# Kernel tuning notes

Measured on AMD Instinct MI355X. Metric: run time of the kernel, lower is better.

The kernel has to match this reference:

```python
import jax, jax.numpy as jnp
import numpy as np

NUM_STEPS = 151            # num_steps from __init__
STEP = 2.0 / (NUM_STEPS - 1)
HALF = (NUM_STEPS - 1) // 2  # bin offset: t_j = -1 + j*STEP, 1/STEP = HALF
N = 4096
D = 512
NUM_CLASSES = 751


def _soft_histogram(s, mask, size):
    # Triangular-kernel (linear) soft binning, equivalent to the original
    # indsa/indsb masked-repeat construction: each similarity s in
    # [t_{j-1}, t_j] contributes (1-frac) to bin j-1 and frac to bin j.
    x = s / STEP
    k = jnp.floor(x)           # zero-gradient, plays the role of s_repeat_floor
    frac = x - k               # (s - (t_j - STEP)) / STEP
    kI = k.astype(jnp.int32)
    idx_lo = jnp.clip(kI + HALF, 0, NUM_STEPS - 1)
    idx_hi = jnp.clip(kI + HALF + 1, 0, NUM_STEPS - 1)
    hist = jnp.zeros((NUM_STEPS,), dtype=s.dtype)
    hist = hist.at[idx_lo].add((1.0 - frac) * mask)
    hist = hist.at[idx_hi].add(frac * mask)
    return hist / size


def setup_inputs() -> dict:
    key = jax.random.key(0)
    kf, kc = jax.random.split(key)
    return {
        "features": jax.random.normal(kf, (N, D), dtype=jnp.float32),
        "classes": jax.random.randint(kc, (N,), 0, NUM_CLASSES, dtype=jnp.int32),
    }


def reference(features, classes):
    # L2Normalization
    f = features / jnp.linalg.norm(features, axis=1, keepdims=True)
    dists = f @ f.T                                   # [N, N] cosine sims
    iu, ju = np.triu_indices(features.shape[0], 1)    # static upper-tri pairs
    s = dists[iu, ju]                                 # [P] P = N(N-1)/2
    pos = (classes[iu] == classes[ju]).astype(s.dtype)
    neg = 1.0 - pos
    hist_pos = _soft_histogram(s, pos, jnp.sum(pos))
    hist_neg = _soft_histogram(s, neg, jnp.sum(neg))
    cdf_pos = jnp.cumsum(hist_pos)                    # tril-masked column sums == cumsum
    return jnp.sum(hist_neg * cdf_pos)
```

## Files before the change

### kernel.cpp

```cpp
#include <hip/hip_runtime.h>
#include <math.h>

#define N 4096
#define D 512
#define NUM_STEPS 151
#define HALF_BINS 75
#define INV_STEP 75.0f
#define NUM_CLASSES 751
#define P_TOTAL 8386560.0f

#define WS_SUM_ALL 0
#define WS_POS_CNT 1
#define WS_SUM_POS 2
#define WS_S_POS   3
#define WS_DONE2   4
#define WS_DONE3   5
#define WS_G_OFF   8
#define WS_H_OFF   160
#define WS_LIST_OFF 1024
#define MAXP (1 << 18)
#define WS_FEAT_OFF (WS_LIST_OFF + MAXP)
#define WS_FEATB_OFF (WS_FEAT_OFF + N * D)
#define WS_IDX_OFF  (WS_FEATB_OFF + N * D / 2)
#define WS_OFFS_OFF (WS_IDX_OFF + N)
#define WS_POFF_OFF (WS_OFFS_OFF + NUM_CLASSES + 1)

#define POS_BLOCKS 512

typedef __bf16 bf16x8 __attribute__((ext_vector_type(8)));
typedef float floatx4 __attribute__((ext_vector_type(4)));

__global__ __launch_bounds__(256) void k_norm_sort(const float* __restrict__ feat,
                                                   const int* __restrict__ cls,
                                                   float* __restrict__ nf,
                                                   __bf16* __restrict__ nfb,
                                                   int* __restrict__ pairList,
                                                   float* __restrict__ wsf,
                                                   int* __restrict__ wsi) {
    int t = threadIdx.x;
    if (blockIdx.x > 0) {
        int row = blockIdx.x - 1;
        const float* fr = feat + (size_t)row * D;
        float a = fr[t];
        float b = fr[t + 256];
        float ss = a * a + b * b;
        for (int o = 32; o > 0; o >>= 1) ss += __shfl_down(ss, o, 64);
        __shared__ float wsum[4];
        int lane = t & 63, wid = t >> 6;
        if (lane == 0) wsum[wid] = ss;
        __syncthreads();
        float tot = wsum[0] + wsum[1] + wsum[2] + wsum[3];
        float inv = 1.0f / sqrtf(tot);
        float na = a * inv, nb = b * inv;
        nf[(size_t)row * D + t] = na;
        nf[(size_t)row * D + t + 256] = nb;
        nfb[(size_t)row * D + t] = (__bf16)na;
        nfb[(size_t)row * D + t + 256] = (__bf16)nb;
        return;
    }

    if (t == 0) {
        wsf[WS_SUM_ALL] = 0.f;
        wsf[WS_SUM_POS] = 0.f;
        wsi[WS_DONE2] = 0;
        wsi[WS_DONE3] = 0;
    }
    {
        float* histG = wsf + WS_H_OFF;
        for (int b = t; b < NUM_STEPS; b += 256) histG[b] = 0.f;
    }
    __shared__ int hcnt[NUM_CLASSES];
    __shared__ int hoff[NUM_CLASSES];
    __shared__ int poff[NUM_CLASSES];
    __shared__ int ridx[N];
    __shared__ int wsumR[4], wsumP[4];
    for (int c = t; c < NUM_CLASSES; c += 256) hcnt[c] = 0;
    __syncthreads();
    for (int n = t; n < N; n += 256) atomicAdd(&hcnt[cls[n]], 1);
    __syncthreads();

    int c0 = t * 3;
    int cntPreR[3], cntPreP[3];
    int myR = 0, myP = 0;
    #pragma unroll
    for (int k = 0; k < 3; ++k) {
        int c = c0 + k;
        int cnt = (c < NUM_CLASSES) ? hcnt[c] : 0;
        cntPreR[k] = myR; cntPreP[k] = myP;
        myR += cnt;
        myP += cnt * (cnt - 1) / 2;
    }
    int lane = t & 63, wv = t >> 6;
    int incR = myR, incP = myP;
    for (int o = 1; o < 64; o <<= 1) {
        int rr = __shfl_up(incR, o, 64);
        int pp = __shfl_up(incP, o, 64);
        if (lane >= o) { incR += rr; incP += pp; }
    }
    if (lane == 63) { wsumR[wv] = incR; wsumP[wv] = incP; }
    __syncthreads();
    int baseR = 0, baseP = 0;
    for (int w = 0; w < wv; ++w) { baseR += wsumR[w]; baseP += wsumP[w]; }
    int exR = baseR + incR - myR;
    int exP = baseP + incP - myP;
    #pragma unroll
    for (int k = 0; k < 3; ++k) {
        int c = c0 + k;
        if (c < NUM_CLASSES) { hoff[c] = exR + cntPreR[k]; poff[c] = exP + cntPreP[k]; }
    }
    __syncthreads();

    for (int c = t; c < NUM_CLASSES; c += 256) hcnt[c] = hoff[c];
    __syncthreads();
    for (int n = t; n < N; n += 256) {
        int p = atomicAdd(&hcnt[cls[n]], 1);
        ridx[p] = n;
    }
    __syncthreads();

    #pragma unroll
    for (int k = 0; k < 3; ++k) {
        int c = c0 + k;
        if (c >= NUM_CLASSES) continue;
        int o0 = hoff[c];
        int nc = hcnt[c] - o0;
        int pB = poff[c];
        int q = 0;
        for (int a = 0; a < nc - 1; ++a) {
            int ri = ridx[o0 + a];
            for (int b = a + 1; b < nc; ++b) {
                int rj = ridx[o0 + b];
                if (pB + q < MAXP) pairList[pB + q] = (ri << 12) | rj;
                ++q;
            }
        }
    }
    if (t == 0) {
        int totP = wsumP[0] + wsumP[1] + wsumP[2] + wsumP[3];
        wsi[WS_POS_CNT] = totP;
    }
}

__global__ __launch_bounds__(256) void k_pos_cdf(const float* __restrict__ nf,
                                                 const int* __restrict__ pairList,
                                                 float* __restrict__ histG,
                                                 float* __restrict__ G,
                                                 float* __restrict__ wsf,
                                                 int* __restrict__ wsi) {
    __shared__ float hloc[NUM_STEPS];
    int t = threadIdx.x;
    int lane = t & 63;
    int wave = t >> 6;
    for (int b = t; b < NUM_STEPS; b += 256) hloc[b] = 0.f;
    __syncthreads();

    int totP = wsi[WS_POS_CNT];
    if (totP > MAXP) totP = MAXP;
    const int STRIDE = POS_BLOCKS * 4;
    int p = blockIdx.x * 4 + wave;
    int vNext = (p < totP) ? pairList[p] : 0;
    for (; p < totP; p += STRIDE) {
        int v = vNext;
        int pn = p + STRIDE;
        if (pn < totP) vNext = pairList[pn];
        int ri = v >> 12, rj = v & 4095;
        const float4* x4 = (const float4*)(nf + (size_t)ri * D);
        const float4* y4 = (const float4*)(nf + (size_t)rj * D);
        float4 xa = x4[lane * 2], xb = x4[lane * 2 + 1];
        float4 ya = y4[lane * 2], yb = y4[lane * 2 + 1];
        float s = xa.x * ya.x + xa.y * ya.y + xa.z * ya.z + xa.w * ya.w
                + xb.x * yb.x + xb.y * yb.y + xb.z * yb.z + xb.w * yb.w;
        for (int o = 32; o > 0; o >>= 1) s += __shfl_down(s, o, 64);
        if (lane == 0) {
            float x = s * INV_STEP;
            float kf = floorf(x);
            float frac = x - kf;
            int kI = (int)kf;
            int lo = min(max(kI + HALF_BINS, 0), NUM_STEPS - 1);
            int hi = min(max(kI + HALF_BINS + 1, 0), NUM_STEPS - 1);
            atomicAdd(&hloc[lo], 1.0f - frac);
            atomicAdd(&hloc[hi], frac);
        }
    }
    __syncthreads();
    for (int b = t; b < NUM_STEPS; b += 256) {
        float v = hloc[b];
        if (v != 0.f) atomicAdd(&histG[b], v);
    }

    __shared__ bool sdone;
    __syncthreads();
    if (t == 0) {
        __threadfence();
        int v = atomicAdd(&wsi[WS_DONE2], 1);
        sdone = (v == (int)gridDim.x - 1);
    }
    __syncthreads();
    if (!sdone) return;

    __shared__ float sc[2][NUM_STEPS];
    float hv = 0.f;
    if (t < NUM_STEPS) {
        hv = atomicAdd(&histG[t], 0.0f);
        sc[0][t] = hv;
    }
    __syncthreads();
    int src = 0;
    for (int o = 1; o < NUM_STEPS; o <<= 1) {
        if (t < NUM_STEPS) {
            float v = sc[src][t];
            if (t >= o) v += sc[src][t - o];
            sc[1 - src][t] = v;
        }
        __syncthreads();
        src ^= 1;
    }
    float invC = (totP > 0) ? (1.0f / (float)totP) : 0.f;
    float prod = 0.f;
    if (t < NUM_STEPS) {
        float g = sc[src][t] * invC;
        G[t] = g;
        prod = hv * g;
    }
    for (int o = 32; o > 0; o >>= 1) prod += __shfl_down(prod, o, 64);
    __shared__ float wsum[4];
    if ((t & 63) == 0) wsum[t >> 6] = prod;
    __syncthreads();
    if (t == 0) {
        wsf[WS_SUM_POS] = wsum[0] + wsum[1] + wsum[2] + wsum[3];
        wsf[WS_S_POS] = (float)totP;
    }
}

#define TILES_1D 32
#define LDSS 40

__global__ __launch_bounds__(256) void k_gram_final(const __bf16* __restrict__ nfb,
                                                    const float* __restrict__ G,
                                                    float* __restrict__ wsf,
                                                    int* __restrict__ wsi,
                                                    float* __restrict__ out) {
    int bid = blockIdx.x;
    int ti = 0, rem = bid;
    while (rem >= TILES_1D - ti) { rem -= TILES_1D - ti; ++ti; }
    int tj = ti + rem;

    __shared__ __align__(16) __bf16 As[128 * LDSS];
    __shared__ __align__(16) __bf16 Bs[128 * LDSS];
    __shared__ float Gs[NUM_STEPS];

    int tid = threadIdx.x;
    for (int b = tid; b < NUM_STEPS; b += 256) Gs[b] = G[b];

    int lane = tid & 63;
    int wave = tid >> 6;
    int wm = (wave >> 1) * 64;
    int wn = (wave & 1) * 64;
    int fr = lane & 15;
    int fk = (lane >> 4) * 8;

    int rowA0 = ti * 128, rowB0 = tj * 128;

    floatx4 acc[4][4] = {};

    int e0 = tid * 8;
    int e1 = e0 + 2048;
    int r0 = e0 >> 5, c0 = e0 & 31;
    int r1 = e1 >> 5, c1 = e1 & 31;

    for (int kb = 0; kb < D / 32; ++kb) {
        int kbase = kb * 32;
        *(float4*)(&As[r0 * LDSS + c0]) = *(const float4*)(nfb + (size_t)(rowA0 + r0) * D + kbase + c0);
        *(float4*)(&As[r1 * LDSS + c1]) = *(const float4*)(nfb + (size_t)(rowA0 + r1) * D + kbase + c1);
        *(float4*)(&Bs[r0 * LDSS + c0]) = *(const float4*)(nfb + (size_t)(rowB0 + r0) * D + kbase + c0);
        *(float4*)(&Bs[r1 * LDSS + c1]) = *(const float4*)(nfb + (size_t)(rowB0 + r1) * D + kbase + c1);
        __syncthreads();

        bf16x8 a[4], b[4];
        #pragma unroll
        for (int r = 0; r < 4; ++r)
            a[r] = *(const bf16x8*)(&As[(wm + r * 16 + fr) * LDSS + fk]);
        #pragma unroll
        for (int c = 0; c < 4; ++c)
            b[c] = *(const bf16x8*)(&Bs[(wn + c * 16 + fr) * LDSS + fk]);

        #pragma unroll
        for (int r = 0; r < 4; ++r)
            #pragma unroll
            for (int c = 0; c < 4; ++c)
                acc[r][c] = __builtin_amdgcn_mfma_f32_16x16x32_bf16(a[r], b[c], acc[r][c], 0, 0, 0);
        __syncthreads();
    }

    int crow = (lane >> 4) * 4;
    int ccol = lane & 15;
    float gsum = 0.f;
    #pragma unroll
    for (int r = 0; r < 4; ++r) {
        #pragma unroll
        for (int c = 0; c < 4; ++c) {
            #pragma unroll
            for (int reg = 0; reg < 4; ++reg) {
                int gi = rowA0 + wm + r * 16 + crow + reg;
                int gj = rowB0 + wn + c * 16 + ccol;
                if (gi < gj) {
                    float s = acc[r][c][reg];
                    float x = s * INV_STEP;
                    float kf = floorf(x);
                    float frac = x - kf;
                    int kI = (int)kf;
                    int lo = min(max(kI + HALF_BINS, 0), NUM_STEPS - 1);
                    int hi = min(max(kI + HALF_BINS + 1, 0), NUM_STEPS - 1);
                    gsum += (1.f - frac) * Gs[lo] + frac * Gs[hi];
                }
            }
        }
    }
    for (int o = 32; o > 0; o >>= 1) gsum += __shfl_down(gsum, o, 64);
    __shared__ float wsum[4];
    if ((tid & 63) == 0) wsum[tid >> 6] = gsum;
    __syncthreads();
    if (tid == 0) atomicAdd(&wsf[WS_SUM_ALL], wsum[0] + wsum[1] + wsum[2] + wsum[3]);

    __shared__ bool sdone;
    if (tid == 0) {
        __threadfence();
        int v = atomicAdd(&wsi[WS_DONE3], 1);
        sdone = (v == (int)gridDim.x - 1);
    }
    __syncthreads();
    if (sdone && tid == 0) {
        __threadfence();
        float sAll = atomicAdd(&wsf[WS_SUM_ALL], 0.0f);
        float C = wsf[WS_S_POS];
        float sneg = P_TOTAL - C;
        out[0] = (sAll - wsf[WS_SUM_POS]) / sneg;
    }
}

extern "C" void kernel_launch(void* const* d_in, const int* in_sizes, int n_in,
                              void* d_out, int out_size, void* d_ws, size_t ws_size,
                              hipStream_t stream) {
    const float* feat = (const float*)d_in[0];
    const int* cls = (const int*)d_in[1];
    float* out = (float*)d_out;
    float* wsf = (float*)d_ws;
    int* wsi = (int*)d_ws;

    float* nf = wsf + WS_FEAT_OFF;
    __bf16* nfb = (__bf16*)(wsf + WS_FEATB_OFF);
    int* pairList = wsi + WS_LIST_OFF;
    float* G = wsf + WS_G_OFF;
    float* histG = wsf + WS_H_OFF;

    k_norm_sort<<<N + 1, 256, 0, stream>>>(feat, cls, nf, nfb, pairList, wsf, wsi);
    k_pos_cdf<<<POS_BLOCKS, 256, 0, stream>>>(nf, pairList, histG, G, wsf, wsi);
    int nTiles = TILES_1D * (TILES_1D + 1) / 2;
    k_gram_final<<<nTiles, 256, 0, stream>>>(nfb, G, wsf, wsi, out);
}
```

Before: 140.0 us.

## Fuse positive-pair histogram and Gram pass into one kernel via all-pair histogram

```diff
diff --git a/kernel.cpp b/kernel.cpp
--- a/kernel.cpp
+++ b/kernel.cpp
@@ -15,17 +15,16 @@
 #define WS_S_POS   3
 #define WS_DONE2   4
 #define WS_DONE3   5
-#define WS_G_OFF   8
-#define WS_H_OFF   160
+#define WS_HP_OFF  8
+#define WS_HA_OFF  160
 #define WS_LIST_OFF 1024
 #define MAXP (1 << 18)
 #define WS_FEAT_OFF (WS_LIST_OFF + MAXP)
 #define WS_FEATB_OFF (WS_FEAT_OFF + N * D)
-#define WS_IDX_OFF  (WS_FEATB_OFF + N * D / 2)
-#define WS_OFFS_OFF (WS_IDX_OFF + N)
-#define WS_POFF_OFF (WS_OFFS_OFF + NUM_CLASSES + 1)
-
-#define POS_BLOCKS 512
+
+#define TILES_1D 32
+#define NTILES (TILES_1D * (TILES_1D + 1) / 2)
+#define LDSS 40
 
 typedef __bf16 bf16x8 __attribute__((ext_vector_type(8)));
 typedef float floatx4 __attribute__((ext_vector_type(4)));
@@ -66,8 +65,10 @@
         wsi[WS_DONE3] = 0;
     }
     {
-        float* histG = wsf + WS_H_OFF;
-        for (int b = t; b < NUM_STEPS; b += 256) histG[b] = 0.f;
+        for (int b = t; b < NUM_STEPS; b += 256) {
+            wsf[WS_HP_OFF + b] = 0.f;
+            wsf[WS_HA_OFF + b] = 0.f;
+        }
     }
     __shared__ int hcnt[NUM_CLASSES];
     __shared__ int hoff[NUM_CLASSES];
@@ -141,119 +142,67 @@
     }
 }
 
-__global__ __launch_bounds__(256) void k_pos_cdf(const float* __restrict__ nf,
-                                                 const int* __restrict__ pairList,
-                                                 float* __restrict__ histG,
-                                                 float* __restrict__ G,
-                                                 float* __restrict__ wsf,
-                                                 int* __restrict__ wsi) {
+__global__ __launch_bounds__(256) void k_pair_gram(const float* __restrict__ nf,
+                                                   const __bf16* __restrict__ nfb,
+                                                   const int* __restrict__ pairList,
+                                                   float* __restrict__ histPosG,
+                                                   float* __restrict__ histAllG,
+                                                   float* __restrict__ wsf,
+                                                   int* __restrict__ wsi,
+                                                   float* __restrict__ out) {
+    __shared__ __align__(16) __bf16 As[128 * LDSS];
+    __shared__ __align__(16) __bf16 Bs[128 * LDSS];
     __shared__ float hloc[NUM_STEPS];
-    int t = threadIdx.x;
-    int lane = t & 63;
-    int wave = t >> 6;
-    for (int b = t; b < NUM_STEPS; b += 256) hloc[b] = 0.f;
+    __shared__ float hAll[NUM_STEPS];
+
+    int tid = threadIdx.x;
+    int lane = tid & 63;
+    int wave = tid >> 6;
+
+    for (int b = tid; b < NUM_STEPS; b += 256) { hloc[b] = 0.f; hAll[b] = 0.f; }
     __syncthreads();
 
     int totP = wsi[WS_POS_CNT];
     if (totP > MAXP) totP = MAXP;
-    const int STRIDE = POS_BLOCKS * 4;
-    int p = blockIdx.x * 4 + wave;
-    int vNext = (p < totP) ? pairList[p] : 0;
-    for (; p < totP; p += STRIDE) {
-        int v = vNext;
-        int pn = p + STRIDE;
-        if (pn < totP) vNext = pairList[pn];
-        int ri = v >> 12, rj = v & 4095;
-        const float4* x4 = (const float4*)(nf + (size_t)ri * D);
-        const float4* y4 = (const float4*)(nf + (size_t)rj * D);
-        float4 xa = x4[lane * 2], xb = x4[lane * 2 + 1];
-        float4 ya = y4[lane * 2], yb = y4[lane * 2 + 1];
-        float s = xa.x * ya.x + xa.y * ya.y + xa.z * ya.z + xa.w * ya.w
-                + xb.x * yb.x + xb.y * yb.y + xb.z * yb.z + xb.w * yb.w;
-        for (int o = 32; o > 0; o >>= 1) s += __shfl_down(s, o, 64);
-        if (lane == 0) {
-            float x = s * INV_STEP;
-            float kf = floorf(x);
-            float frac = x - kf;
-            int kI = (int)kf;
-            int lo = min(max(kI + HALF_BINS, 0), NUM_STEPS - 1);
-            int hi = min(max(kI + HALF_BINS + 1, 0), NUM_STEPS - 1);
-            atomicAdd(&hloc[lo], 1.0f - frac);
-            atomicAdd(&hloc[hi], frac);
-        }
-    }
-    __syncthreads();
-    for (int b = t; b < NUM_STEPS; b += 256) {
+    {
+        const int STRIDE = NTILES * 4;
+        int p = blockIdx.x * 4 + wave;
+        int vNext = (p < totP) ? pairList[p] : 0;
+        for (; p < totP; p += STRIDE) {
+            int v = vNext;
+            int pn = p + STRIDE;
+            if (pn < totP) vNext = pairList[pn];
+            int ri = v >> 12, rj = v & 4095;
+            const float4* x4 = (const float4*)(nf + (size_t)ri * D);
+            const float4* y4 = (const float4*)(nf + (size_t)rj * D);
+            float4 xa = x4[lane * 2], xb = x4[lane * 2 + 1];
+            float4 ya = y4[lane * 2], yb = y4[lane * 2 + 1];
+            float s = xa.x * ya.x + xa.y * ya.y + xa.z * ya.z + xa.w * ya.w
+                    + xb.x * yb.x + xb.y * yb.y + xb.z * yb.z + xb.w * yb.w;
+            for (int o = 32; o > 0; o >>= 1) s += __shfl_down(s, o, 64);
+            if (lane == 0) {
+                float x = s * INV_STEP;
+                float kf = floorf(x);
+                float frac = x - kf;
+                int kI = (int)kf;
+                int lo = min(max(kI + HALF_BINS, 0), NUM_STEPS - 1);
+                int hi = min(max(kI + HALF_BINS + 1, 0), NUM_STEPS - 1);
+                atomicAdd(&hloc[lo], 1.0f - frac);
+                atomicAdd(&hloc[hi], frac);
+            }
+        }
+    }
+    __syncthreads();
+    for (int b = tid; b < NUM_STEPS; b += 256) {
         float v = hloc[b];
-        if (v != 0.f) atomicAdd(&histG[b], v);
-    }
-
-    __shared__ bool sdone;
-    __syncthreads();
-    if (t == 0) {
-        __threadfence();
-        int v = atomicAdd(&wsi[WS_DONE2], 1);
-        sdone = (v == (int)gridDim.x - 1);
-    }
-    __syncthreads();
-    if (!sdone) return;
-
-    __shared__ float sc[2][NUM_STEPS];
-    float hv = 0.f;
-    if (t < NUM_STEPS) {
-        hv = atomicAdd(&histG[t], 0.0f);
-        sc[0][t] = hv;
-    }
-    __syncthreads();
-    int src = 0;
-    for (int o = 1; o < NUM_STEPS; o <<= 1) {
-        if (t < NUM_STEPS) {
-            float v = sc[src][t];
-            if (t >= o) v += sc[src][t - o];
-            sc[1 - src][t] = v;
-        }
-        __syncthreads();
-        src ^= 1;
-    }
-    float invC = (totP > 0) ? (1.0f / (float)totP) : 0.f;
-    float prod = 0.f;
-    if (t < NUM_STEPS) {
-        float g = sc[src][t] * invC;
-        G[t] = g;
-        prod = hv * g;
-    }
-    for (int o = 32; o > 0; o >>= 1) prod += __shfl_down(prod, o, 64);
-    __shared__ float wsum[4];
-    if ((t & 63) == 0) wsum[t >> 6] = prod;
-    __syncthreads();
-    if (t == 0) {
-        wsf[WS_SUM_POS] = wsum[0] + wsum[1] + wsum[2] + wsum[3];
-        wsf[WS_S_POS] = (float)totP;
-    }
-}
-
-#define TILES_1D 32
-#define LDSS 40
-
-__global__ __launch_bounds__(256) void k_gram_final(const __bf16* __restrict__ nfb,
-                                                    const float* __restrict__ G,
-                                                    float* __restrict__ wsf,
-                                                    int* __restrict__ wsi,
-                                                    float* __restrict__ out) {
+        if (v != 0.f) atomicAdd(&histPosG[b], v);
+    }
+
     int bid = blockIdx.x;
     int ti = 0, rem = bid;
     while (rem >= TILES_1D - ti) { rem -= TILES_1D - ti; ++ti; }
     int tj = ti + rem;
 
-    __shared__ __align__(16) __bf16 As[128 * LDSS];
-    __shared__ __align__(16) __bf16 Bs[128 * LDSS];
-    __shared__ float Gs[NUM_STEPS];
-
-    int tid = threadIdx.x;
-    for (int b = tid; b < NUM_STEPS; b += 256) Gs[b] = G[b];
-
-    int lane = tid & 63;
-    int wave = tid >> 6;
     int wm = (wave >> 1) * 64;
     int wn = (wave & 1) * 64;
     int fr = lane & 15;
@@ -294,7 +243,6 @@
 
     int crow = (lane >> 4) * 4;
     int ccol = lane & 15;
-    float gsum = 0.f;
     #pragma unroll
     for (int r = 0; r < 4; ++r) {
         #pragma unroll
@@ -311,31 +259,58 @@
                     int kI = (int)kf;
                     int lo = min(max(kI + HALF_BINS, 0), NUM_STEPS - 1);
                     int hi = min(max(kI + HALF_BINS + 1, 0), NUM_STEPS - 1);
-                    gsum += (1.f - frac) * Gs[lo] + frac * Gs[hi];
+                    atomicAdd(&hAll[lo], 1.0f - frac);
+                    atomicAdd(&hAll[hi], frac);
                 }
             }
         }
     }
-    for (int o = 32; o > 0; o >>= 1) gsum += __shfl_down(gsum, o, 64);
-    __shared__ float wsum[4];
-    if ((tid & 63) == 0) wsum[tid >> 6] = gsum;
-    __syncthreads();
-    if (tid == 0) atomicAdd(&wsf[WS_SUM_ALL], wsum[0] + wsum[1] + wsum[2] + wsum[3]);
+    __syncthreads();
+    for (int b = tid; b < NUM_STEPS; b += 256) {
+        float v = hAll[b];
+        if (v != 0.f) atomicAdd(&histAllG[b], v);
+    }
 
     __shared__ bool sdone;
+    __threadfence();
+    __syncthreads();
     if (tid == 0) {
-        __threadfence();
         int v = atomicAdd(&wsi[WS_DONE3], 1);
         sdone = (v == (int)gridDim.x - 1);
     }
     __syncthreads();
-    if (sdone && tid == 0) {
-        __threadfence();
-        float sAll = atomicAdd(&wsf[WS_SUM_ALL], 0.0f);
-        float C = wsf[WS_S_POS];
-        float sneg = P_TOTAL - C;
-        out[0] = (sAll - wsf[WS_SUM_POS]) / sneg;
-    }
+    if (!sdone) return;
+
+    float hp = 0.f, ha = 0.f;
+    if (tid < NUM_STEPS) {
+        hp = atomicAdd(&histPosG[tid], 0.0f);
+        ha = atomicAdd(&histAllG[tid], 0.0f);
+    }
+    __shared__ float sc[2][NUM_STEPS];
+    if (tid < NUM_STEPS) sc[0][tid] = hp;
+    __syncthreads();
+    int src = 0;
+    for (int o = 1; o < NUM_STEPS; o <<= 1) {
+        if (tid < NUM_STEPS) {
+            float v = sc[src][tid];
+            if (tid >= o) v += sc[src][tid - o];
+            sc[1 - src][tid] = v;
+        }
+        __syncthreads();
+        src ^= 1;
+    }
+    float invC = (totP > 0) ? (1.0f / (float)totP) : 0.f;
+    float sneg = P_TOTAL - (float)totP;
+    float term = 0.f;
+    if (tid < NUM_STEPS) {
+        float g = sc[src][tid] * invC;
+        term = ((ha - hp) / sneg) * g;
+    }
+    for (int o = 32; o > 0; o >>= 1) term += __shfl_down(term, o, 64);
+    __shared__ float wsum[4];
+    if ((tid & 63) == 0) wsum[tid >> 6] = term;
+    __syncthreads();
+    if (tid == 0) out[0] = wsum[0] + wsum[1] + wsum[2] + wsum[3];
 }
 
 extern "C" void kernel_launch(void* const* d_in, const int* in_sizes, int n_in,
@@ -350,11 +325,10 @@
     float* nf = wsf + WS_FEAT_OFF;
     __bf16* nfb = (__bf16*)(wsf + WS_FEATB_OFF);
     int* pairList = wsi + WS_LIST_OFF;
-    float* G = wsf + WS_G_OFF;
-    float* histG = wsf + WS_H_OFF;
+    float* histPosG = wsf + WS_HP_OFF;
+    float* histAllG = wsf + WS_HA_OFF;
 
     k_norm_sort<<<N + 1, 256, 0, stream>>>(feat, cls, nf, nfb, pairList, wsf, wsi);
-    k_pos_cdf<<<POS_BLOCKS, 256, 0, stream>>>(nf, pairList, histG, G, wsf, wsi);
-    int nTiles = TILES_1D * (TILES_1D + 1) / 2;
-    k_gram_final<<<nTiles, 256, 0, stream>>>(nfb, G, wsf, wsi, out);
+    k_pair_gram<<<NTILES, 256, 0, stream>>>(nf, nfb, pairList, histPosG, histAllG,
+                                            wsf, wsi, out);
 }
```

Result: slower. 255.7 us (+82.6%).

## Use direct global-to-LDS loads with BK=64 in gram kernel, batch normalization rows

Applied to the files above, without the earlier changes.

```diff
diff --git a/kernel.cpp b/kernel.cpp
--- a/kernel.cpp
+++ b/kernel.cpp
@@ -21,14 +21,17 @@
 #define MAXP (1 << 18)
 #define WS_FEAT_OFF (WS_LIST_OFF + MAXP)
 #define WS_FEATB_OFF (WS_FEAT_OFF + N * D)
-#define WS_IDX_OFF  (WS_FEATB_OFF + N * D / 2)
-#define WS_OFFS_OFF (WS_IDX_OFF + N)
-#define WS_POFF_OFF (WS_OFFS_OFF + NUM_CLASSES + 1)
 
 #define POS_BLOCKS 512
 
 typedef __bf16 bf16x8 __attribute__((ext_vector_type(8)));
+typedef __bf16 bf16x4 __attribute__((ext_vector_type(4)));
 typedef float floatx4 __attribute__((ext_vector_type(4)));
+
+__device__ __forceinline__ void gload16(const void* g, void* l) {
+    __builtin_amdgcn_global_load_lds((const __attribute__((address_space(1))) void*)g,
+                                     (__attribute__((address_space(3))) void*)l, 16, 0, 0);
+}
 
 __global__ __launch_bounds__(256) void k_norm_sort(const float* __restrict__ feat,
                                                    const int* __restrict__ cls,
@@ -39,23 +42,28 @@
                                                    int* __restrict__ wsi) {
     int t = threadIdx.x;
     if (blockIdx.x > 0) {
-        int row = blockIdx.x - 1;
-        const float* fr = feat + (size_t)row * D;
-        float a = fr[t];
-        float b = fr[t + 256];
-        float ss = a * a + b * b;
-        for (int o = 32; o > 0; o >>= 1) ss += __shfl_down(ss, o, 64);
-        __shared__ float wsum[4];
-        int lane = t & 63, wid = t >> 6;
-        if (lane == 0) wsum[wid] = ss;
-        __syncthreads();
-        float tot = wsum[0] + wsum[1] + wsum[2] + wsum[3];
-        float inv = 1.0f / sqrtf(tot);
-        float na = a * inv, nb = b * inv;
-        nf[(size_t)row * D + t] = na;
-        nf[(size_t)row * D + t + 256] = nb;
-        nfb[(size_t)row * D + t] = (__bf16)na;
-        nfb[(size_t)row * D + t + 256] = (__bf16)nb;
+        int lane = t & 63;
+        int wave = t >> 6;
+        int rowBase = (((int)blockIdx.x - 1) * 4 + wave) * 4;
+        #pragma unroll
+        for (int i = 0; i < 4; ++i) {
+            int row = rowBase + i;
+            const float4* x4 = (const float4*)(feat + (size_t)row * D);
+            float4 xa = x4[lane];
+            float4 xb = x4[lane + 64];
+            float ss = xa.x * xa.x + xa.y * xa.y + xa.z * xa.z + xa.w * xa.w
+                     + xb.x * xb.x + xb.y * xb.y + xb.z * xb.z + xb.w * xb.w;
+            for (int o = 32; o > 0; o >>= 1) ss += __shfl_xor(ss, o, 64);
+            float inv = 1.0f / sqrtf(ss);
+            float4 na = make_float4(xa.x * inv, xa.y * inv, xa.z * inv, xa.w * inv);
+            float4 nb = make_float4(xb.x * inv, xb.y * inv, xb.z * inv, xb.w * inv);
+            ((float4*)(nf + (size_t)row * D))[lane] = na;
+            ((float4*)(nf + (size_t)row * D))[lane + 64] = nb;
+            bf16x4 v0 = { (__bf16)na.x, (__bf16)na.y, (__bf16)na.z, (__bf16)na.w };
+            bf16x4 v1 = { (__bf16)nb.x, (__bf16)nb.y, (__bf16)nb.z, (__bf16)nb.w };
+            *(bf16x4*)(nfb + (size_t)row * D + lane * 4) = v0;
+            *(bf16x4*)(nfb + (size_t)row * D + 256 + lane * 4) = v1;
+        }
         return;
     }
 
@@ -65,10 +73,8 @@
         wsi[WS_DONE2] = 0;
         wsi[WS_DONE3] = 0;
     }
-    {
-        float* histG = wsf + WS_H_OFF;
-        for (int b = t; b < NUM_STEPS; b += 256) histG[b] = 0.f;
-    }
+    for (int b = t; b < NUM_STEPS; b += 256) wsf[WS_H_OFF + b] = 0.f;
+
     __shared__ int hcnt[NUM_CLASSES];
     __shared__ int hoff[NUM_CLASSES];
     __shared__ int poff[NUM_CLASSES];
@@ -233,7 +239,8 @@
 }
 
 #define TILES_1D 32
-#define LDSS 40
+#define NTILES (TILES_1D * (TILES_1D + 1) / 2)
+#define BK 64
 
 __global__ __launch_bounds__(256) void k_gram_final(const __bf16* __restrict__ nfb,
                                                     const float* __restrict__ G,
@@ -245,8 +252,8 @@
     while (rem >= TILES_1D - ti) { rem -= TILES_1D - ti; ++ti; }
     int tj = ti + rem;
 
-    __shared__ __align__(16) __bf16 As[128 * LDSS];
-    __shared__ __align__(16) __bf16 Bs[128 * LDSS];
+    __shared__ __align__(16) __bf16 As[128 * BK];
+    __shared__ __align__(16) __bf16 Bs[128 * BK];
     __shared__ float Gs[NUM_STEPS];
 
     int tid = threadIdx.x;
@@ -261,34 +268,40 @@
 
     int rowA0 = ti * 128, rowB0 = tj * 128;
 
+    int srow = wave * 32 + (lane >> 3);
+    int scol = (lane & 7) * 8;
+
     floatx4 acc[4][4] = {};
 
-    int e0 = tid * 8;
-    int e1 = e0 + 2048;
-    int r0 = e0 >> 5, c0 = e0 & 31;
-    int r1 = e1 >> 5, c1 = e1 & 31;
-
-    for (int kb = 0; kb < D / 32; ++kb) {
-        int kbase = kb * 32;
-        *(float4*)(&As[r0 * LDSS + c0]) = *(const float4*)(nfb + (size_t)(rowA0 + r0) * D + kbase + c0);
-        *(float4*)(&As[r1 * LDSS + c1]) = *(const float4*)(nfb + (size_t)(rowA0 + r1) * D + kbase + c1);
-        *(float4*)(&Bs[r0 * LDSS + c0]) = *(const float4*)(nfb + (size_t)(rowB0 + r0) * D + kbase + c0);
-        *(float4*)(&Bs[r1 * LDSS + c1]) = *(const float4*)(nfb + (size_t)(rowB0 + r1) * D + kbase + c1);
+    for (int kb = 0; kb < D / BK; ++kb) {
+        int kbase = kb * BK;
+        #pragma unroll
+        for (int c = 0; c < 4; ++c) {
+            gload16(nfb + (size_t)(rowA0 + srow + c * 8) * D + kbase + scol,
+                    &As[(wave * 32 + c * 8) * BK]);
+        }
+        #pragma unroll
+        for (int c = 0; c < 4; ++c) {
+            gload16(nfb + (size_t)(rowB0 + srow + c * 8) * D + kbase + scol,
+                    &Bs[(wave * 32 + c * 8) * BK]);
+        }
         __syncthreads();
 
-        bf16x8 a[4], b[4];
-        #pragma unroll
-        for (int r = 0; r < 4; ++r)
-            a[r] = *(const bf16x8*)(&As[(wm + r * 16 + fr) * LDSS + fk]);
-        #pragma unroll
-        for (int c = 0; c < 4; ++c)
-            b[c] = *(const bf16x8*)(&Bs[(wn + c * 16 + fr) * LDSS + fk]);
-
-        #pragma unroll
-        for (int r = 0; r < 4; ++r)
+        #pragma unroll
+        for (int kk = 0; kk < 2; ++kk) {
+            bf16x8 a[4], b[4];
+            #pragma unroll
+            for (int r = 0; r < 4; ++r)
+                a[r] = *(const bf16x8*)(&As[(wm + r * 16 + fr) * BK + kk * 32 + fk]);
             #pragma unroll
             for (int c = 0; c < 4; ++c)
-                acc[r][c] = __builtin_amdgcn_mfma_f32_16x16x32_bf16(a[r], b[c], acc[r][c], 0, 0, 0);
+                b[c] = *(const bf16x8*)(&Bs[(wn + c * 16 + fr) * BK + kk * 32 + fk]);
+            #pragma unroll
+            for (int r = 0; r < 4; ++r)
+                #pragma unroll
+                for (int c = 0; c < 4; ++c)
+                    acc[r][c] = __builtin_amdgcn_mfma_f32_16x16x32_bf16(a[r], b[c], acc[r][c], 0, 0, 0);
+        }
         __syncthreads();
     }
 
@@ -353,8 +366,7 @@
     float* G = wsf + WS_G_OFF;
     float* histG = wsf + WS_H_OFF;
 
-    k_norm_sort<<<N + 1, 256, 0, stream>>>(feat, cls, nf, nfb, pairList, wsf, wsi);
+    k_norm_sort<<<257, 256, 0, stream>>>(feat, cls, nf, nfb, pairList, wsf, wsi);
     k_pos_cdf<<<POS_BLOCKS, 256, 0, stream>>>(nf, pairList, histG, G, wsf, wsi);
-    int nTiles = TILES_1D * (TILES_1D + 1) / 2;
-    k_gram_final<<<nTiles, 256, 0, stream>>>(nfb, G, wsf, wsi, out);
-}
+    k_gram_final<<<NTILES, 256, 0, stream>>>(nfb, G, wsf, wsi, out);
+}
```

Result: slower. 153.0 us (+9.3%).
